# Performance work log

Hardware: AMD Instinct MI355X
Metric: run time of the kernel (lower is better)

Reference implementation:

```python
import jax, jax.numpy as jnp
import numpy as np

A = 1.0  # slope of hard sigmoid (init arg `a`)


def setup_inputs() -> dict:
    key = jax.random.key(0)
    ks = jax.random.split(key, 10)
    H, B, BOT, TOP = 1024, 4096, 1024, 1024
    stdv = 1.0 / np.sqrt(H)
    u = lambda k, shp: jax.random.uniform(k, shp, jnp.float32, -stdv, stdv)
    U_11 = u(ks[0], (4 * H + 1, H))
    U_21 = u(ks[1], (4 * H + 1, TOP))
    W_01 = u(ks[2], (4 * H + 1, BOT))
    bias = u(ks[3], (4 * H + 1,))
    c = jax.random.normal(ks[4], (H, B), jnp.float32) * 0.1
    h = jnp.tanh(jax.random.normal(ks[5], (H, B), jnp.float32))
    h_bottom = jnp.tanh(jax.random.normal(ks[6], (BOT, B), jnp.float32))
    h_top = jnp.tanh(jax.random.normal(ks[7], (TOP, B), jnp.float32))
    z = (jax.random.uniform(ks[8], (1, B)) > 0.5).astype(jnp.float32)
    z_bottom = (jax.random.uniform(ks[9], (1, B)) > 0.5).astype(jnp.float32)
    return dict(c=c, h_bottom=h_bottom, h=h, h_top=h_top, z=z,
                z_bottom=z_bottom, U_11=U_11, U_21=U_21, W_01=W_01, bias=bias)


def reference(c, h_bottom, h, h_top, z, z_bottom, U_11, U_21, W_01, bias):
    H = U_11.shape[1]
    # [4H+1, B] pre-activations: recurrent + gated top-down + gated bottom-up + bias
    f_s = (W_01 @ h_bottom
           + z * (U_21 @ h_top)
           + z_bottom * (U_11 @ h)
           + bias[:, None])
    f = jax.nn.sigmoid(f_s[0:H])
    i = jax.nn.sigmoid(f_s[H:2 * H])
    o = jax.nn.sigmoid(f_s[2 * H:3 * H])
    g = jnp.tanh(f_s[3 * H:4 * H])
    z_hat = jnp.clip((f_s[4 * H:4 * H + 1] * A + 1.0) / 2.0, 0.0, 1.0)  # hard_sigm
    one = 1.0
    c_new = (z * (i * g)
             + (one - z) * (one - z_bottom) * c
             + (one - z) * z_bottom * (f * c + i * g))
    tanh_c = jnp.tanh(c_new)
    h_new = (z * o * tanh_c
             + (one - z) * (one - z_bottom) * h
             + (one - z) * z_bottom * o * tanh_c)
    # straight-through binary boundary: forward step(z_hat>0.5), backward identity
    z_new = z_hat + jax.lax.stop_gradient((z_hat > 0.5).astype(z_hat.dtype) - z_hat)
    return h_new, c_new, z_new
```

## Files before the change

### kernel.cpp

```cpp
#include <hip/hip_runtime.h>
#include <hip/hip_bf16.h>
#include <math.h>

#define Hd   1024
#define Bsz  4096
#define Kc   3072
#define NT   48

typedef unsigned short u16;
typedef __attribute__((ext_vector_type(8))) u16 u16x8;
typedef __attribute__((ext_vector_type(2))) u16 u16x2;
typedef __attribute__((ext_vector_type(16))) float f32x16;
typedef __attribute__((ext_vector_type(8))) short bf16x8;

template<bool V> struct BoolC { static constexpr bool value = V; };

__device__ inline u16 f2bf(float f) {
    __hip_bfloat16 h = __float2bfloat16(f);
    return *reinterpret_cast<u16*>(&h);
}

__device__ inline float sigm(float x) { return 1.0f / (1.0f + __expf(-x)); }

__device__ inline void gload16(const void* g, const void* s) {
    __builtin_amdgcn_global_load_lds(
        (const __attribute__((address_space(1))) void*)g,
        (__attribute__((address_space(3))) void*)s, 16, 0, 0);
}

#define BAR()   __builtin_amdgcn_s_barrier()
#define VMW(n)  asm volatile("s_waitcnt vmcnt(" #n ")" ::: "memory")

__global__ __launch_bounds__(256) void prep_A(const float* __restrict__ U11,
                                              const float* __restrict__ U21,
                                              const float* __restrict__ W01,
                                              u16* __restrict__ Ab,
                                              float* __restrict__ out) {
    if (blockIdx.x == 0) {
        float* outz = out + (size_t)2 * Hd * Bsz;
        for (int i = threadIdx.x; i < Bsz; i += 256) outz[i] = 0.0f;
    }
    int t = blockIdx.x * 256 + threadIdx.x;
    int row = t / 384;
    int kc = (t - row * 384) * 8;
    int r = row >> 2, gate = row & 3;
    int sel = kc >> 10;
    int k = kc & 1023;
    const float* src = (sel == 0) ? W01 : ((sel == 1) ? U21 : U11);
    const float4* p = reinterpret_cast<const float4*>(src + (size_t)(gate * Hd + r) * Hd + k);
    float4 v0 = p[0], v1 = p[1];
    u16x8 o;
    o[0] = f2bf(v0.x); o[1] = f2bf(v0.y); o[2] = f2bf(v0.z); o[3] = f2bf(v0.w);
    o[4] = f2bf(v1.x); o[5] = f2bf(v1.y); o[6] = f2bf(v1.z); o[7] = f2bf(v1.w);
    *reinterpret_cast<u16x8*>(Ab + (size_t)row * Kc + kc) = o;
}

__global__ __launch_bounds__(256) void prep_B(const float* __restrict__ hb,
                                              const float* __restrict__ ht,
                                              const float* __restrict__ hh,
                                              const float* __restrict__ z,
                                              const float* __restrict__ zb,
                                              const float* __restrict__ U11,
                                              const float* __restrict__ U21,
                                              const float* __restrict__ W01,
                                              u16* __restrict__ Bb,
                                              float* __restrict__ out) {
    __shared__ float tile[64][33];
    __shared__ float red[8][32];
    int n0 = blockIdx.x * 32;
    int kg0 = blockIdx.y * 64;
    int sel = kg0 >> 10;
    int k0 = kg0 & 1023;
    const float* src = (sel == 0) ? hb : ((sel == 1) ? ht : hh);
    const float* wsrc = (sel == 0) ? W01 : ((sel == 1) ? U21 : U11);
    int t = threadIdx.x, tx = t & 31, ty = t >> 5;
#pragma unroll
    for (int j = 0; j < 8; ++j) {
        int kk = ty * 8 + j;
        tile[kk][tx] = src[(size_t)(k0 + kk) * Bsz + n0 + tx];
    }
    __syncthreads();
    {
        int kp = t & 31, ny = t >> 5;
#pragma unroll
        for (int j = 0; j < 4; ++j) {
            int nl = ny * 4 + j;
            int n = n0 + nl;
            float s = (sel == 0) ? 1.0f : ((sel == 1) ? z[n] : zb[n]);
            u16x2 o;
            o[0] = f2bf(tile[kp * 2][nl] * s);
            o[1] = f2bf(tile[kp * 2 + 1][nl] * s);
            *reinterpret_cast<u16x2*>(Bb + (size_t)n * Kc + kg0 + kp * 2) = o;
        }
    }
    {
        int col = t & 31, seg = t >> 5;
        const float* w = wsrc + (size_t)4096 * 1024 + k0 + seg * 8;
        float p = 0.0f;
#pragma unroll
        for (int j = 0; j < 8; ++j) p += w[j] * tile[seg * 8 + j][col];
        red[seg][col] = p;
        __syncthreads();
        if (seg == 0) {
            float tot = 0.0f;
#pragma unroll
            for (int q = 0; q < 8; ++q) tot += red[q][col];
            int n = n0 + col;
            float sca = (sel == 0) ? 1.0f : ((sel == 1) ? z[n] : zb[n]);
            atomicAdd(out + (size_t)2 * Hd * Bsz + n, tot * sca);
        }
    }
}

__global__ __launch_bounds__(512, 2) void gemm_fused(
    const u16* __restrict__ A, const u16* __restrict__ Bm,
    const float* __restrict__ c_in, const float* __restrict__ h_in,
    const float* __restrict__ z, const float* __restrict__ zb,
    const float* __restrict__ bias, float* __restrict__ out) {
    extern __shared__ __align__(16) u16 smem[];
    u16* const AsB = smem;
    u16* const BsB = smem + 32768;

    const int t = threadIdx.x;
    const int w = t >> 6, l = t & 63;
    const int wm = w >> 2, wn = w & 3;
    const int c = l & 31, hi = l >> 5, key = l & 7;

    const int orig = blockIdx.x;
    const int wg = ((orig & 7) << 5) | (orig >> 3);
    const int bm = wg >> 4, bn = wg & 15;

    const int srow = t >> 3;
    const int sgs  = (t & 7) ^ (srow & 7);

    f32x16 accum[4][2];
#pragma unroll
    for (int i = 0; i < 4; ++i)
#pragma unroll
        for (int j = 0; j < 2; ++j)
#pragma unroll
            for (int e = 0; e < 16; ++e) accum[i][j][e] = 0.0f;

    const u16* gA = A  + (size_t)(bm * 256 + srow) * Kc + sgs * 8;
    const u16* gB = Bm + (size_t)(bn * 256 + srow) * Kc + sgs * 8;

    auto stageA = [&](int buf, int half, int kt) {
#pragma unroll
        for (int iss = 0; iss < 2; ++iss) {
            const u16* g = gA + (size_t)(half * 128 + iss * 64) * Kc + kt * 64;
            const u16* d = AsB + buf * 16384 + (half * 128 + iss * 64 + (w << 3)) * 64;
            gload16(g, d);
        }
    };
    auto stageB = [&](int buf, int half, int kt) {
#pragma unroll
        for (int iss = 0; iss < 2; ++iss) {
            const u16* g = gB + (size_t)(half * 128 + iss * 64) * Kc + kt * 64;
            const u16* d = BsB + buf * 16384 + (half * 128 + iss * 64 + (w << 3)) * 64;
            gload16(g, d);
        }
    };

    bf16x8 aF[2][2][4];
    bf16x8 bQ0[4], bQ1[4];

    auto rdA = [&](const u16* base, int mh, int mb, int ks) -> bf16x8 {
        int row = mh * 128 + wm * 64 + mb * 32 + c;
        int slot = (2 * ks + hi) ^ key;
        return *reinterpret_cast<const bf16x8*>(base + row * 64 + slot * 8);
    };
    auto rdB = [&](const u16* base, int nh, int ks) -> bf16x8 {
        int row = nh * 128 + wn * 32 + c;
        int slot = (2 * ks + hi) ^ key;
        return *reinterpret_cast<const bf16x8*>(base + row * 64 + slot * 8);
    };

    stageA(0, 0, 0); stageB(0, 0, 0); stageA(0, 1, 0); stageB(0, 1, 0);
    VMW(2); BAR();

    auto ktile = [&](int tc, auto pfc) {
        constexpr bool pf = decltype(pfc)::value;
        const int cur = tc & 1, nxt = cur ^ 1;
        const u16* Ac = AsB + cur * 16384;
        const u16* Bc = BsB + cur * 16384;
        if constexpr (pf) stageA(nxt, 0, tc + 1);
#pragma unroll
        for (int mb = 0; mb < 2; ++mb)
#pragma unroll
            for (int ks = 0; ks < 4; ++ks) aF[0][mb][ks] = rdA(Ac, 0, mb, ks);
#pragma unroll
        for (int ks = 0; ks < 4; ++ks) bQ0[ks] = rdB(Bc, 0, ks);
#pragma unroll
        for (int mb = 0; mb < 2; ++mb)
#pragma unroll
            for (int ks = 0; ks < 4; ++ks) aF[1][mb][ks] = rdA(Ac, 1, mb, ks);
        BAR();
        __builtin_amdgcn_s_setprio(1);
#pragma unroll
        for (int mb = 0; mb < 2; ++mb)
#pragma unroll
            for (int ks = 0; ks < 4; ++ks)
                accum[mb][0] = __builtin_amdgcn_mfma_f32_32x32x16_bf16(
                    aF[0][mb][ks], bQ0[ks], accum[mb][0], 0, 0, 0);
        __builtin_amdgcn_s_setprio(0);
        if constexpr (pf) { VMW(2); } else { VMW(0); }
        BAR();
        if constexpr (pf) stageB(nxt, 0, tc + 1);
#pragma unroll
        for (int ks = 0; ks < 4; ++ks) bQ1[ks] = rdB(Bc, 1, ks);
        BAR();
        __builtin_amdgcn_s_setprio(1);
#pragma unroll
        for (int mb = 0; mb < 2; ++mb)
#pragma unroll
            for (int ks = 0; ks < 4; ++ks)
                accum[2 + mb][0] = __builtin_amdgcn_mfma_f32_32x32x16_bf16(
                    aF[1][mb][ks], bQ0[ks], accum[2 + mb][0], 0, 0, 0);
        __builtin_amdgcn_s_setprio(0);
        BAR();
        if constexpr (pf) stageA(nxt, 1, tc + 1);
        BAR();
        __builtin_amdgcn_s_setprio(1);
#pragma unroll
        for (int mb = 0; mb < 2; ++mb)
#pragma unroll
            for (int ks = 0; ks < 4; ++ks)
                accum[2 + mb][1] = __builtin_amdgcn_mfma_f32_32x32x16_bf16(
                    aF[1][mb][ks], bQ1[ks], accum[2 + mb][1], 0, 0, 0);
        __builtin_amdgcn_s_setprio(0);
        BAR();
        if constexpr (pf) stageB(nxt, 1, tc + 1);
        BAR();
        __builtin_amdgcn_s_setprio(1);
#pragma unroll
        for (int mb = 0; mb < 2; ++mb)
#pragma unroll
            for (int ks = 0; ks < 4; ++ks)
                accum[mb][1] = __builtin_amdgcn_mfma_f32_32x32x16_bf16(
                    aF[0][mb][ks], bQ1[ks], accum[mb][1], 0, 0, 0);
        __builtin_amdgcn_s_setprio(0);
        if constexpr (pf) { VMW(2); }
        BAR();
    };

    for (int tc = 0; tc < NT - 1; ++tc) ktile(tc, BoolC<true>{});
    ktile(NT - 1, BoolC<false>{});

    float zc[2], zbv[2];
#pragma unroll
    for (int nh = 0; nh < 2; ++nh) {
        int n = bn * 256 + nh * 128 + wn * 32 + c;
        zc[nh] = z[n]; zbv[nh] = zb[n];
    }
#pragma unroll
    for (int mh = 0; mh < 2; ++mh)
#pragma unroll
        for (int mb = 0; mb < 2; ++mb) {
            const int u0 = bm * 64 + mh * 32 + wm * 16 + mb * 8;
#pragma unroll
            for (int nh = 0; nh < 2; ++nh) {
                const int n = bn * 256 + nh * 128 + wn * 32 + c;
                const float zcv = zc[nh], zbvv = zbv[nh];
                const float nz = 1.0f - zcv, nzb = 1.0f - zbvv;
                f32x16 a = accum[mh * 2 + mb][nh];
#pragma unroll
                for (int q = 0; q < 4; ++q) {
                    const int r = u0 + 2 * q + hi;
                    const float co = c_in[(size_t)r * Bsz + n];
                    const float ho = h_in[(size_t)r * Bsz + n];
                    float fg = sigm(a[4 * q + 0] + bias[r]);
                    float ig = sigm(a[4 * q + 1] + bias[Hd + r]);
                    float og = sigm(a[4 * q + 2] + bias[2 * Hd + r]);
                    float gg = tanhf(a[4 * q + 3] + bias[3 * Hd + r]);
                    float i_g = ig * gg;
                    float cn = zcv * i_g + nz * nzb * co + nz * zbvv * (fg * co + i_g);
                    float tc2 = tanhf(cn);
                    float hn = zcv * og * tc2 + nz * nzb * ho + nz * zbvv * og * tc2;
                    out[(size_t)r * Bsz + n] = hn;
                    out[(size_t)Hd * Bsz + (size_t)r * Bsz + n] = cn;
                }
            }
        }

    if (bm == 0 && t < 256) {
        float* outz = out + (size_t)2 * Hd * Bsz;
        int n = bn * 256 + t;
        float s = outz[n] + bias[4096];
        float zh = (s + 1.0f) * 0.5f;
        zh = fminf(fmaxf(zh, 0.0f), 1.0f);
        outz[n] = (zh > 0.5f) ? 1.0f : 0.0f;
    }
}

extern "C" void kernel_launch(void* const* d_in, const int* in_sizes, int n_in,
                              void* d_out, int out_size, void* d_ws, size_t ws_size,
                              hipStream_t stream) {
    (void)in_sizes; (void)n_in; (void)out_size; (void)ws_size;
    const float* c    = (const float*)d_in[0];
    const float* hb   = (const float*)d_in[1];
    const float* h    = (const float*)d_in[2];
    const float* ht   = (const float*)d_in[3];
    const float* z    = (const float*)d_in[4];
    const float* zb   = (const float*)d_in[5];
    const float* U11  = (const float*)d_in[6];
    const float* U21  = (const float*)d_in[7];
    const float* W01  = (const float*)d_in[8];
    const float* bias = (const float*)d_in[9];
    float* out = (float*)d_out;

    u16* Ab = (u16*)d_ws;
    u16* Bb = Ab + (size_t)4096 * Kc;

    hipFuncSetAttribute(reinterpret_cast<const void*>(gemm_fused),
                        hipFuncAttributeMaxDynamicSharedMemorySize, 131072);

    prep_A<<<6144, 256, 0, stream>>>(U11, U21, W01, Ab, out);
    prep_B<<<dim3(128, 48), 256, 0, stream>>>(hb, ht, h, z, zb, U11, U21, W01, Bb, out);
    gemm_fused<<<256, 512, 131072, stream>>>(Ab, Bb, c, h, z, zb, bias, out);
}
```

Before: 139.1 us.

## Pre-tile bf16 operands into MFMA fragment order and simplify the K-loop schedule

The prep kernels now write A and B in a blocked layout ordered by 32-row block, k-tile, k-step and half, so each MFMA fragment is a contiguous 256-element chunk. The GEMM stages whole contiguous 4 KB chunks with global_load_lds and reads LDS fragments without XOR swizzling. The k-loop is also rewritten with fewer barriers and different vmcnt waits, still double buffered. LDS reads of c*8 with a 16-byte stride per lane may now hit bank conflicts, and the new wait counts could be off.

```diff
diff --git a/kernel.cpp b/kernel.cpp
--- a/kernel.cpp
+++ b/kernel.cpp
@@ -13,8 +13,6 @@
 typedef __attribute__((ext_vector_type(16))) float f32x16;
 typedef __attribute__((ext_vector_type(8))) short bf16x8;
 
-template<bool V> struct BoolC { static constexpr bool value = V; };
-
 __device__ inline u16 f2bf(float f) {
     __hip_bfloat16 h = __float2bfloat16(f);
     return *reinterpret_cast<u16*>(&h);
@@ -30,6 +28,9 @@
 
 #define BAR()   __builtin_amdgcn_s_barrier()
 #define VMW(n)  asm volatile("s_waitcnt vmcnt(" #n ")" ::: "memory")
+#define PRIO1() __builtin_amdgcn_s_setprio(1)
+#define PRIO0() __builtin_amdgcn_s_setprio(0)
+
 
 __global__ __launch_bounds__(256) void prep_A(const float* __restrict__ U11,
                                               const float* __restrict__ U21,
@@ -52,7 +53,10 @@
     u16x8 o;
     o[0] = f2bf(v0.x); o[1] = f2bf(v0.y); o[2] = f2bf(v0.z); o[3] = f2bf(v0.w);
     o[4] = f2bf(v1.x); o[5] = f2bf(v1.y); o[6] = f2bf(v1.z); o[7] = f2bf(v1.w);
-    *reinterpret_cast<u16x8*>(Ab + (size_t)row * Kc + kc) = o;
+    int mb = row >> 5, r32 = row & 31;
+    int kt = kc >> 6, ks = (kc >> 4) & 3, hi = (kc >> 3) & 1;
+    size_t off = ((((size_t)mb * NT + kt) * 4 + ks) * 2 + hi) * 256 + r32 * 8;
+    *reinterpret_cast<u16x8*>(Ab + off) = o;
 }
 
 __global__ __launch_bounds__(256) void prep_B(const float* __restrict__ hb,
@@ -82,6 +86,11 @@
     __syncthreads();
     {
         int kp = t & 31, ny = t >> 5;
+        const int nb = n0 >> 5;
+        const int kt = kg0 >> 6;
+        const int kk2 = kp * 2;
+        const int ks = kk2 >> 4, hi2 = (kk2 >> 3) & 1, e = kk2 & 7;
+        const size_t base = ((((size_t)nb * NT + kt) * 4 + ks) * 2 + hi2) * 256 + e;
 #pragma unroll
         for (int j = 0; j < 4; ++j) {
             int nl = ny * 4 + j;
@@ -90,7 +99,7 @@
             u16x2 o;
             o[0] = f2bf(tile[kp * 2][nl] * s);
             o[1] = f2bf(tile[kp * 2 + 1][nl] * s);
-            *reinterpret_cast<u16x2*>(Bb + (size_t)n * Kc + kg0 + kp * 2) = o;
+            *reinterpret_cast<u16x2*>(Bb + base + nl * 8) = o;
         }
     }
     {
@@ -124,127 +133,94 @@
     const int t = threadIdx.x;
     const int w = t >> 6, l = t & 63;
     const int wm = w >> 2, wn = w & 3;
-    const int c = l & 31, hi = l >> 5, key = l & 7;
+    const int c = l & 31, hi = l >> 5;
 
     const int orig = blockIdx.x;
     const int wg = ((orig & 7) << 5) | (orig >> 3);
     const int bm = wg >> 4, bn = wg & 15;
 
-    const int srow = t >> 3;
-    const int sgs  = (t & 7) ^ (srow & 7);
-
-    f32x16 accum[4][2];
+    f32x16 acc[4][2];
 #pragma unroll
     for (int i = 0; i < 4; ++i)
 #pragma unroll
         for (int j = 0; j < 2; ++j)
 #pragma unroll
-            for (int e = 0; e < 16; ++e) accum[i][j][e] = 0.0f;
-
-    const u16* gA = A  + (size_t)(bm * 256 + srow) * Kc + sgs * 8;
-    const u16* gB = Bm + (size_t)(bn * 256 + srow) * Kc + sgs * 8;
+            for (int e = 0; e < 16; ++e) acc[i][j][e] = 0.0f;
 
     auto stageA = [&](int buf, int half, int kt) {
 #pragma unroll
         for (int iss = 0; iss < 2; ++iss) {
-            const u16* g = gA + (size_t)(half * 128 + iss * 64) * Kc + kt * 64;
-            const u16* d = AsB + buf * 16384 + (half * 128 + iss * 64 + (w << 3)) * 64;
+            size_t mbg = (size_t)(bm * 8 + half * 4 + iss * 2 + (t >> 8));
+            const u16* g = A + (mbg * NT + kt) * 2048 + (t & 255) * 8;
+            const u16* d = AsB + buf * 16384 + half * 8192 + iss * 4096 + t * 8;
             gload16(g, d);
         }
     };
     auto stageB = [&](int buf, int half, int kt) {
 #pragma unroll
         for (int iss = 0; iss < 2; ++iss) {
-            const u16* g = gB + (size_t)(half * 128 + iss * 64) * Kc + kt * 64;
-            const u16* d = BsB + buf * 16384 + (half * 128 + iss * 64 + (w << 3)) * 64;
+            size_t nbg = (size_t)(bn * 8 + half * 4 + iss * 2 + (t >> 8));
+            const u16* g = Bm + (nbg * NT + kt) * 2048 + (t & 255) * 8;
+            const u16* d = BsB + buf * 16384 + half * 8192 + iss * 4096 + t * 8;
             gload16(g, d);
         }
     };
 
     bf16x8 aF[2][2][4];
-    bf16x8 bQ0[4], bQ1[4];
-
-    auto rdA = [&](const u16* base, int mh, int mb, int ks) -> bf16x8 {
-        int row = mh * 128 + wm * 64 + mb * 32 + c;
-        int slot = (2 * ks + hi) ^ key;
-        return *reinterpret_cast<const bf16x8*>(base + row * 64 + slot * 8);
-    };
-    auto rdB = [&](const u16* base, int nh, int ks) -> bf16x8 {
-        int row = nh * 128 + wn * 32 + c;
-        int slot = (2 * ks + hi) ^ key;
-        return *reinterpret_cast<const bf16x8*>(base + row * 64 + slot * 8);
-    };
+    bf16x8 bF[2][4];
+
+    auto readA = [&](int buf, int mh, int mb, int ks) -> bf16x8 {
+        return *reinterpret_cast<const bf16x8*>(
+            AsB + buf * 16384 + mh * 8192 + (wm * 2 + mb) * 2048 +
+            (ks * 2 + hi) * 256 + c * 8);
+    };
+    auto readB = [&](int buf, int nh, int ks) -> bf16x8 {
+        return *reinterpret_cast<const bf16x8*>(
+            BsB + buf * 16384 + nh * 8192 + wn * 2048 +
+            (ks * 2 + hi) * 256 + c * 8);
+    };
+
+#define MFMAQ(mh, nh)                                                         \
+    PRIO1();                                                                  \
+    _Pragma("unroll")                                                         \
+    for (int mb = 0; mb < 2; ++mb)                                            \
+        _Pragma("unroll")                                                     \
+        for (int ks = 0; ks < 4; ++ks)                                        \
+            acc[(mh)*2 + mb][nh] = __builtin_amdgcn_mfma_f32_32x32x16_bf16(   \
+                aF[mh][mb][ks], bF[nh][ks], acc[(mh)*2 + mb][nh], 0, 0, 0);   \
+    PRIO0()
 
     stageA(0, 0, 0); stageB(0, 0, 0); stageA(0, 1, 0); stageB(0, 1, 0);
-    VMW(2); BAR();
-
-    auto ktile = [&](int tc, auto pfc) {
-        constexpr bool pf = decltype(pfc)::value;
-        const int cur = tc & 1, nxt = cur ^ 1;
-        const u16* Ac = AsB + cur * 16384;
-        const u16* Bc = BsB + cur * 16384;
-        if constexpr (pf) stageA(nxt, 0, tc + 1);
+    VMW(3); BAR();
+
+    for (int T = 0; T < NT; ++T) {
+        const int p = T & 1, q2 = p ^ 1;
+        const bool more = (T + 1 < NT);
 #pragma unroll
         for (int mb = 0; mb < 2; ++mb)
 #pragma unroll
-            for (int ks = 0; ks < 4; ++ks) aF[0][mb][ks] = rdA(Ac, 0, mb, ks);
-#pragma unroll
-        for (int ks = 0; ks < 4; ++ks) bQ0[ks] = rdB(Bc, 0, ks);
+            for (int ks = 0; ks < 4; ++ks) aF[0][mb][ks] = readA(p, 0, mb, ks);
+#pragma unroll
+        for (int ks = 0; ks < 4; ++ks) bF[0][ks] = readB(p, 0, ks);
+        if (more) { stageA(q2, 0, T + 1); VMW(3); } else { VMW(2); }
+        BAR();
+        MFMAQ(0, 0);
 #pragma unroll
         for (int mb = 0; mb < 2; ++mb)
 #pragma unroll
-            for (int ks = 0; ks < 4; ++ks) aF[1][mb][ks] = rdA(Ac, 1, mb, ks);
-        BAR();
-        __builtin_amdgcn_s_setprio(1);
-#pragma unroll
-        for (int mb = 0; mb < 2; ++mb)
-#pragma unroll
-            for (int ks = 0; ks < 4; ++ks)
-                accum[mb][0] = __builtin_amdgcn_mfma_f32_32x32x16_bf16(
-                    aF[0][mb][ks], bQ0[ks], accum[mb][0], 0, 0, 0);
-        __builtin_amdgcn_s_setprio(0);
-        if constexpr (pf) { VMW(2); } else { VMW(0); }
-        BAR();
-        if constexpr (pf) stageB(nxt, 0, tc + 1);
-#pragma unroll
-        for (int ks = 0; ks < 4; ++ks) bQ1[ks] = rdB(Bc, 1, ks);
-        BAR();
-        __builtin_amdgcn_s_setprio(1);
-#pragma unroll
-        for (int mb = 0; mb < 2; ++mb)
-#pragma unroll
-            for (int ks = 0; ks < 4; ++ks)
-                accum[2 + mb][0] = __builtin_amdgcn_mfma_f32_32x32x16_bf16(
-                    aF[1][mb][ks], bQ0[ks], accum[2 + mb][0], 0, 0, 0);
-        __builtin_amdgcn_s_setprio(0);
-        BAR();
-        if constexpr (pf) stageA(nxt, 1, tc + 1);
-        BAR();
-        __builtin_amdgcn_s_setprio(1);
-#pragma unroll
-        for (int mb = 0; mb < 2; ++mb)
-#pragma unroll
-            for (int ks = 0; ks < 4; ++ks)
-                accum[2 + mb][1] = __builtin_amdgcn_mfma_f32_32x32x16_bf16(
-                    aF[1][mb][ks], bQ1[ks], accum[2 + mb][1], 0, 0, 0);
-        __builtin_amdgcn_s_setprio(0);
-        BAR();
-        if constexpr (pf) stageB(nxt, 1, tc + 1);
-        BAR();
-        __builtin_amdgcn_s_setprio(1);
-#pragma unroll
-        for (int mb = 0; mb < 2; ++mb)
-#pragma unroll
-            for (int ks = 0; ks < 4; ++ks)
-                accum[mb][1] = __builtin_amdgcn_mfma_f32_32x32x16_bf16(
-                    aF[0][mb][ks], bQ1[ks], accum[mb][1], 0, 0, 0);
-        __builtin_amdgcn_s_setprio(0);
-        if constexpr (pf) { VMW(2); }
-        BAR();
-    };
-
-    for (int tc = 0; tc < NT - 1; ++tc) ktile(tc, BoolC<true>{});
-    ktile(NT - 1, BoolC<false>{});
+            for (int ks = 0; ks < 4; ++ks) aF[1][mb][ks] = readA(p, 1, mb, ks);
+        if (more) { stageB(q2, 0, T + 1); VMW(3); } else { VMW(0); }
+        BAR();
+        MFMAQ(1, 0);
+#pragma unroll
+        for (int ks = 0; ks < 4; ++ks) bF[1][ks] = readB(p, 1, ks);
+        if (more) stageA(q2, 1, T + 1);
+        BAR();
+        MFMAQ(1, 1);
+        if (more) { stageB(q2, 1, T + 1); VMW(3); }
+        BAR();
+        MFMAQ(0, 1);
+    }
 
     float zc[2], zbv[2];
 #pragma unroll
@@ -262,7 +238,7 @@
                 const int n = bn * 256 + nh * 128 + wn * 32 + c;
                 const float zcv = zc[nh], zbvv = zbv[nh];
                 const float nz = 1.0f - zcv, nzb = 1.0f - zbvv;
-                f32x16 a = accum[mh * 2 + mb][nh];
+                f32x16 a = acc[mh * 2 + mb][nh];
 #pragma unroll
                 for (int q = 0; q < 4; ++q) {
                     const int r = u0 + 2 * q + hi;
@@ -290,6 +266,7 @@
         zh = fminf(fmaxf(zh, 0.0f), 1.0f);
         outz[n] = (zh > 0.5f) ? 1.0f : 0.0f;
     }
+#undef MFMAQ
 }
 
 extern "C" void kernel_launch(void* const* d_in, const int* in_sizes, int n_in,
```

Result: slower. 145.3 us (+4.5%).
